# Performance work log

Hardware: AMD Instinct MI355X
Metric: run time of the kernel (lower is better)

Reference implementation:

```python
import jax, jax.numpy as jnp
import numpy as np

B, T, L, H, W, D = 16, 4096, 4, 128, 128, 32  # batch, points, views, plane HxW, c_dim
MAX_DIM = 0.55


def _linear_init(key, fan_in, fan_out):
    k1, k2 = jax.random.split(key)
    bound = 1.0 / np.sqrt(fan_in)
    Wm = jax.random.uniform(k1, (fan_in, fan_out), minval=-bound, maxval=bound, dtype=jnp.float32)
    b = jax.random.uniform(k2, (fan_out,), minval=-bound, maxval=bound, dtype=jnp.float32)
    return Wm, b


def setup_inputs() -> dict:
    key = jax.random.key(0)
    ks = jax.random.split(key, 10)
    p = jax.random.uniform(ks[0], (B, T, 3), dtype=jnp.float32, minval=-0.5, maxval=0.5)
    z = jax.random.normal(ks[1], (B, 128), dtype=jnp.float32)
    c = jax.random.normal(ks[2], (B, L, H, W, D), dtype=jnp.float32)
    C_mat = jax.random.normal(ks[3], (B, L, 4, 3), dtype=jnp.float32)
    fc_p_W, fc_p_b = _linear_init(ks[4], 3, D)
    # 5 ResnetBlockFC blocks, each with fc_0 and fc_1 (D->D)
    W0s, b0s, W1s, b1s = [], [], [], []
    for i in range(5):
        kk = jax.random.split(ks[5 + (i % 4)], 2 * (i + 1))
        w0, bb0 = _linear_init(jax.random.fold_in(key, 100 + i), D, D)
        w1, bb1 = _linear_init(jax.random.fold_in(key, 200 + i), D, D)
        W0s.append(w0); b0s.append(bb0); W1s.append(w1); b1s.append(bb1)
    blocks_W0 = jnp.stack(W0s); blocks_b0 = jnp.stack(b0s)
    blocks_W1 = jnp.stack(W1s); blocks_b1 = jnp.stack(b1s)
    fc_out_W, fc_out_b = _linear_init(ks[9], D, 1)
    return {
        'p': p, 'z': z, 'c': c, 'C_mat': C_mat,
        'fc_p_W': fc_p_W, 'fc_p_b': fc_p_b,
        'blocks_W0': blocks_W0, 'blocks_b0': blocks_b0,
        'blocks_W1': blocks_W1, 'blocks_b1': blocks_b1,
        'fc_out_W': fc_out_W, 'fc_out_b': fc_out_b,
    }


def bilinear_interpolation(p, net, C_mat):
    # p: [B,T,3]; net: [B,L,H,W,D]; C_mat: [B,L,4,3]
    Bb, Ll, Hh, Ww, Dd = net.shape
    interval = 2.0 / (Hh - 1)
    # project points with all views at once: C[:, l, :3] @ p^T, vectorized over l
    proj = jnp.einsum('blij,btj->blti', C_mat[:, :, :3, :], p / MAX_DIM)  # [B,L,T,3]
    proj = proj / (C_mat[:, :, 3, 0] + 0.05)[:, :, None, None]
    xy = (proj[..., :2] + 1.0) / interval  # [B,L,T,2]
    xy = jnp.where(xy >= Hh - 1, Hh - 1 - 0.1, xy)
    xy = jnp.where(xy < 0, 0.0, xy)
    xg, yg = xy[..., 0], xy[..., 1]  # [B,L,T]
    # torch.round and jnp.round both round half-to-even
    xl = jnp.round(xg - 0.5); xr = jnp.round(xg + 0.5)
    yl = jnp.round(yg - 0.5); yh = jnp.round(yg + 0.5)
    xi_l = xl.astype(jnp.int32); xi_r = xr.astype(jnp.int32)
    yi_l = yl.astype(jnp.int32); yi_h = yh.astype(jnp.int32)
    bi = jnp.arange(Bb)[:, None, None]
    li = jnp.arange(Ll)[None, :, None]
    f11 = net[bi, li, xi_l, yi_l]  # [B,L,T,D]
    f12 = net[bi, li, xi_r, yi_l]
    f21 = net[bi, li, xi_l, yi_h]
    f22 = net[bi, li, xi_r, yi_h]
    dx = (xr - xg)[..., None]
    dy = (yh - yg)[..., None]
    feat = f11 * dx * dy + f12 * (1 - dx) * dy + f21 * dx * (1 - dy) + f22 * (1 - dx) * (1 - dy)
    return jnp.sum(feat, axis=1)  # sum over views -> [B,T,D]


def resnet_block(x, W0, b0, W1, b1):
    # ResnetBlockFC(size_in == size_out): x + fc_1(relu(fc_0(relu(x))))
    h = jax.nn.relu(x) @ W0 + b0
    dx = jax.nn.relu(h) @ W1 + b1
    return x + dx


def reference(p, z, c, C_mat, fc_p_W, fc_p_b, blocks_W0, blocks_b0, blocks_W1, blocks_b1, fc_out_W, fc_out_b):
    cf = bilinear_interpolation(p, c, C_mat)  # [B,T,D]
    net = p @ fc_p_W + fc_p_b  # [B,T,D]
    net = net + cf
    net = resnet_block(net, blocks_W0[0], blocks_b0[0], blocks_W1[0], blocks_b1[0])
    for i in range(1, 5):
        net = net + cf
        net = resnet_block(net, blocks_W0[i], blocks_b0[i], blocks_W1[i], blocks_b1[i])
    out = jax.nn.relu(net) @ fc_out_W + fc_out_b  # [B,T,1]
    return out[..., 0]
```

## Files before the change

kernel.cpp:

```cpp
#include <hip/hip_runtime.h>
#include <hip/hip_bf16.h>


#define LL 4
#define HH 128
#define WW 128
#define DD 32
#define NPT 65536

typedef __attribute__((ext_vector_type(8))) short bf16x8t;
typedef __attribute__((ext_vector_type(4))) float f32x4;

union ABfrag { bf16x8t v; unsigned u[4]; };

__device__ __forceinline__ unsigned pk2(float a, float b) {
    __hip_bfloat16 ha = __float2bfloat16(a);
    __hip_bfloat16 hb = __float2bfloat16(b);
    unsigned short ua = *reinterpret_cast<unsigned short*>(&ha);
    unsigned short ub = *reinterpret_cast<unsigned short*>(&hb);
    return (unsigned)ua | ((unsigned)ub << 16);
}

__global__ __launch_bounds__(512, 2) void decoder_fused_mfma(
    const float* __restrict__ p,
    const float* __restrict__ c,
    const float* __restrict__ Cmat,
    const float* __restrict__ fc_p_W,
    const float* __restrict__ fc_p_b,
    const float* __restrict__ W0,
    const float* __restrict__ b0,
    const float* __restrict__ W1,
    const float* __restrict__ b1,
    const float* __restrict__ fc_out_W,
    const float* __restrict__ fc_out_b,
    float* __restrict__ out)
{
    __shared__ float xb[4608];

    const int tid = threadIdx.x;

    const int i    = blockIdx.x;
    const int b_u  = (i & 7) + ((i >> 8) << 3);
    const int blk  = (i >> 3) & 31;
    const int tbase = b_u * 4096 + blk * 128;

    const float inv_maxdim   = 1.0f / 0.55f;
    const float inv_interval = 1.0f / (float)(2.0 / 127.0);

    {
        const int tl = tid >> 2;
        const int dg = tid & 3;
        const int t  = tbase + tl;

        const float* pp = p + (size_t)t * 3;
        const float pm0 = pp[0] * inv_maxdim;
        const float pm1 = pp[1] * inv_maxdim;
        const float pm2 = pp[2] * inv_maxdim;

        float acc[8];
        #pragma unroll
        for (int ii = 0; ii < 8; ++ii) acc[ii] = 0.0f;

        #pragma unroll
        for (int l = 0; l < LL; ++l) {
            const float* cm = Cmat + (size_t)(b_u * LL + l) * 12;
            const float c00 = cm[0], c01 = cm[1], c02 = cm[2];
            const float c10 = cm[3], c11 = cm[4], c12 = cm[5];
            const float c30 = cm[9];

            float pr0 = c00 * pm0 + c01 * pm1 + c02 * pm2;
            float pr1 = c10 * pm0 + c11 * pm1 + c12 * pm2;
            const float denom = c30 + 0.05f;
            pr0 = pr0 / denom;
            pr1 = pr1 / denom;

            float xg = (pr0 + 1.0f) * inv_interval;
            float yg = (pr1 + 1.0f) * inv_interval;
            xg = (xg >= 127.0f) ? 126.9f : xg;
            xg = (xg < 0.0f)    ? 0.0f   : xg;
            yg = (yg >= 127.0f) ? 126.9f : yg;
            yg = (yg < 0.0f)    ? 0.0f   : yg;

            const float xl = rintf(xg - 0.5f);
            const float xr = rintf(xg + 0.5f);
            const float yl = rintf(yg - 0.5f);
            const float yh = rintf(yg + 0.5f);
            const int xil = (int)xl, xir = (int)xr, yil = (int)yl, yih = (int)yh;

            const float dx = xr - xg;
            const float dy = yh - yg;
            const float w11 = dx * dy;
            const float w12 = (1.0f - dx) * dy;
            const float w21 = dx * (1.0f - dy);
            const float w22 = (1.0f - dx) * (1.0f - dy);

            const float* plane = c + (size_t)(b_u * LL + l) * (HH * WW * DD);
            const int doff = dg * 8;
            const float* t11 = plane + ((size_t)xil * WW + yil) * DD + doff;
            const float* t12 = plane + ((size_t)xir * WW + yil) * DD + doff;
            const float* t21 = plane + ((size_t)xil * WW + yih) * DD + doff;
            const float* t22 = plane + ((size_t)xir * WW + yih) * DD + doff;

            #pragma unroll
            for (int hf = 0; hf < 2; ++hf) {
                const float4 a  = *(const float4*)(t11 + 4 * hf);
                const float4 e  = *(const float4*)(t12 + 4 * hf);
                const float4 g  = *(const float4*)(t21 + 4 * hf);
                const float4 d4 = *(const float4*)(t22 + 4 * hf);
                acc[4*hf + 0] += w11 * a.x + w12 * e.x + w21 * g.x + w22 * d4.x;
                acc[4*hf + 1] += w11 * a.y + w12 * e.y + w21 * g.y + w22 * d4.y;
                acc[4*hf + 2] += w11 * a.z + w12 * e.z + w21 * g.z + w22 * d4.z;
                acc[4*hf + 3] += w11 * a.w + w12 * e.w + w21 * g.w + w22 * d4.w;
            }
        }

        float* dst = xb + tl * 36 + dg * 8;
        *(float4*)(dst)     = make_float4(acc[0], acc[1], acc[2], acc[3]);
        *(float4*)(dst + 4) = make_float4(acc[4], acc[5], acc[6], acc[7]);
    }
    __syncthreads();

    const int lane = tid & 63;
    const int wv   = tid >> 6;
    const int cch  = lane & 15;
    const int q    = lane >> 4;
    const int tl0  = wv * 16;
    const int tpt  = tbase + tl0;

    f32x4 cf0, cf1;
    #pragma unroll
    for (int r = 0; r < 4; ++r) {
        const int ptl = tl0 + q * 4 + r;
        cf0[r] = xb[ptl * 36 + cch];
        cf1[r] = xb[ptl * 36 + 16 + cch];
    }

    const float fpb0 = fc_p_b[cch],        fpb1 = fc_p_b[16 + cch];
    const float fw00 = fc_p_W[cch],        fw01 = fc_p_W[16 + cch];
    const float fw10 = fc_p_W[DD + cch],   fw11 = fc_p_W[DD + 16 + cch];
    const float fw20 = fc_p_W[2*DD + cch], fw21 = fc_p_W[2*DD + 16 + cch];

    f32x4 net0, net1;
    #pragma unroll
    for (int r = 0; r < 4; ++r) {
        const int pt = tpt + q * 4 + r;
        const float* pp = p + (size_t)pt * 3;
        const float px = pp[0], py = pp[1], pz = pp[2];
        net0[r] = fpb0 + px * fw00 + py * fw10 + pz * fw20 + cf0[r];
        net1[r] = fpb1 + px * fw01 + py * fw11 + pz * fw21 + cf1[r];
    }

    __syncthreads();
    float* myxb = xb + wv * 576;

    #pragma unroll
    for (int s = 0; s < 5; ++s) {
        unsigned wB[2][2][4];
        #pragma unroll
        for (int m = 0; m < 2; ++m) {
            const float* Wm = (m ? W1 : W0) + s * DD * DD;
            #pragma unroll
            for (int tile = 0; tile < 2; ++tile) {
                const float* base = Wm + tile * 16 + cch;
                #pragma unroll
                for (int ii = 0; ii < 4; ++ii) {
                    const float wlo = base[(8 * q + 2 * ii)     * DD];
                    const float whi = base[(8 * q + 2 * ii + 1) * DD];
                    wB[m][tile][ii] = pk2(wlo, whi);
                }
            }
        }
        const float bc00 = b0[s * DD + cch];
        const float bc01 = b0[s * DD + 16 + cch];
        const float bc10 = b1[s * DD + cch];
        const float bc11 = b1[s * DD + 16 + cch];

        if (s > 0) {
            #pragma unroll
            for (int r = 0; r < 4; ++r) { net0[r] += cf0[r]; net1[r] += cf1[r]; }
        }

        #pragma unroll
        for (int r = 0; r < 4; ++r) {
            myxb[(q * 4 + r) * 36 + cch]      = fmaxf(net0[r], 0.0f);
            myxb[(q * 4 + r) * 36 + 16 + cch] = fmaxf(net1[r], 0.0f);
        }
        __syncthreads();
        ABfrag A1;
        {
            const float* row = myxb + cch * 36 + 8 * q;
            const f32x4 alo = *(const f32x4*)(row);
            const f32x4 ahi = *(const f32x4*)(row + 4);
            A1.u[0] = pk2(alo[0], alo[1]);
            A1.u[1] = pk2(alo[2], alo[3]);
            A1.u[2] = pk2(ahi[0], ahi[1]);
            A1.u[3] = pk2(ahi[2], ahi[3]);
        }
        __syncthreads();

        f32x4 h0 = { bc00, bc00, bc00, bc00 };
        f32x4 h1 = { bc01, bc01, bc01, bc01 };
        {
            ABfrag B0a, B0b;
            #pragma unroll
            for (int ii = 0; ii < 4; ++ii) { B0a.u[ii] = wB[0][0][ii]; B0b.u[ii] = wB[0][1][ii]; }
            h0 = __builtin_amdgcn_mfma_f32_16x16x32_bf16(A1.v, B0a.v, h0, 0, 0, 0);
            h1 = __builtin_amdgcn_mfma_f32_16x16x32_bf16(A1.v, B0b.v, h1, 0, 0, 0);
        }

        #pragma unroll
        for (int r = 0; r < 4; ++r) {
            myxb[(q * 4 + r) * 36 + cch]      = fmaxf(h0[r], 0.0f);
            myxb[(q * 4 + r) * 36 + 16 + cch] = fmaxf(h1[r], 0.0f);
        }
        __syncthreads();
        ABfrag A2;
        {
            const float* row = myxb + cch * 36 + 8 * q;
            const f32x4 alo = *(const f32x4*)(row);
            const f32x4 ahi = *(const f32x4*)(row + 4);
            A2.u[0] = pk2(alo[0], alo[1]);
            A2.u[1] = pk2(alo[2], alo[3]);
            A2.u[2] = pk2(ahi[0], ahi[1]);
            A2.u[3] = pk2(ahi[2], ahi[3]);
        }
        __syncthreads();

        #pragma unroll
        for (int r = 0; r < 4; ++r) { net0[r] += bc10; net1[r] += bc11; }
        {
            ABfrag B1a, B1b;
            #pragma unroll
            for (int ii = 0; ii < 4; ++ii) { B1a.u[ii] = wB[1][0][ii]; B1b.u[ii] = wB[1][1][ii]; }
            net0 = __builtin_amdgcn_mfma_f32_16x16x32_bf16(A2.v, B1a.v, net0, 0, 0, 0);
            net1 = __builtin_amdgcn_mfma_f32_16x16x32_bf16(A2.v, B1b.v, net1, 0, 0, 0);
        }
    }

    const float wo0 = fc_out_W[cch];
    const float wo1 = fc_out_W[16 + cch];
    float acc[4];
    #pragma unroll
    for (int r = 0; r < 4; ++r)
        acc[r] = fmaxf(net0[r], 0.0f) * wo0 + fmaxf(net1[r], 0.0f) * wo1;
    #pragma unroll
    for (int m = 1; m < 16; m <<= 1) {
        #pragma unroll
        for (int r = 0; r < 4; ++r) acc[r] += __shfl_xor(acc[r], m, 64);
    }
    if (cch == 0) {
        const float ob = fc_out_b[0];
        #pragma unroll
        for (int r = 0; r < 4; ++r) out[tpt + q * 4 + r] = acc[r] + ob;
    }
}

extern "C" void kernel_launch(void* const* d_in, const int* in_sizes, int n_in,
                              void* d_out, int out_size, void* d_ws, size_t ws_size,
                              hipStream_t stream) {
    const float* p        = (const float*)d_in[0];
    const float* c        = (const float*)d_in[2];
    const float* Cmat     = (const float*)d_in[3];
    const float* fc_p_W   = (const float*)d_in[4];
    const float* fc_p_b   = (const float*)d_in[5];
    const float* W0       = (const float*)d_in[6];
    const float* b0       = (const float*)d_in[7];
    const float* W1       = (const float*)d_in[8];
    const float* b1       = (const float*)d_in[9];
    const float* fc_out_W = (const float*)d_in[10];
    const float* fc_out_b = (const float*)d_in[11];
    float* out = (float*)d_out;

    decoder_fused_mfma<<<NPT / 128, 512, 0, stream>>>(p, c, Cmat, fc_p_W, fc_p_b,
                                                      W0, b0, W1, b1, fc_out_W, fc_out_b, out);
}
```

Measured before the change: 208.0 us.

## Stage packed MLP weights in LDS and replace block barriers with wave-local fences

The bf16-packed weight fragments and biases for all five residual blocks are now built once per workgroup into shared-memory tables, instead of every wave re-reading and re-packing them from global memory at each stage. The scaled point coordinates are also cached in shared memory, so the fc_p step no longer reloads p from global memory. Each stage's block-wide __syncthreads pairs become a single s_waitcnt lgkmcnt(0). This relies on each wave touching only its own 16-row slice of the scratch buffer. The cost is extra LDS (about 23 KB of tables), which may limit occupancy, and the correctness depends on wave-local LDS ordering.

```diff
diff --git a/kernel.cpp b/kernel.cpp
--- a/kernel.cpp
+++ b/kernel.cpp
@@ -19,6 +19,10 @@
     unsigned short ua = *reinterpret_cast<unsigned short*>(&ha);
     unsigned short ub = *reinterpret_cast<unsigned short*>(&hb);
     return (unsigned)ua | ((unsigned)ub << 16);
+}
+
+__device__ __forceinline__ void lds_fence() {
+    asm volatile("s_waitcnt lgkmcnt(0)" ::: "memory");
 }
 
 __global__ __launch_bounds__(512, 2) void decoder_fused_mfma(
@@ -35,7 +39,9 @@
     const float* __restrict__ fc_out_b,
     float* __restrict__ out)
 {
-    __shared__ float xb[4608];
+    __shared__ __align__(16) float xb[4608];
+    __shared__ uint4 wtab[1280];
+    __shared__ float btab[640];
 
     const int tid = threadIdx.x;
 
@@ -47,6 +53,25 @@
     const float inv_maxdim   = 1.0f / 0.55f;
     const float inv_interval = 1.0f / (float)(2.0 / 127.0);
 
+    for (int f = tid; f < 1280; f += 512) {
+        const int ln   = f & 63;
+        const int idx  = f >> 6;
+        const int tile = idx & 1;
+        const int m    = (idx >> 1) & 1;
+        const int s    = idx >> 2;
+        const int cchf = ln & 15;
+        const int qf   = ln >> 4;
+        const float* base = (m ? W1 : W0) + s * DD * DD + tile * 16 + cchf;
+        uint4 w;
+        w.x = pk2(base[(8 * qf + 0) * DD], base[(8 * qf + 1) * DD]);
+        w.y = pk2(base[(8 * qf + 2) * DD], base[(8 * qf + 3) * DD]);
+        w.z = pk2(base[(8 * qf + 4) * DD], base[(8 * qf + 5) * DD]);
+        w.w = pk2(base[(8 * qf + 6) * DD], base[(8 * qf + 7) * DD]);
+        wtab[f] = w;
+    }
+    for (int f = tid; f < 640; f += 512)
+        btab[f] = (f < 320) ? b0[f] : b1[f - 320];
+
     {
         const int tl = tid >> 2;
         const int dg = tid & 3;
@@ -56,6 +81,12 @@
         const float pm0 = pp[0] * inv_maxdim;
         const float pm1 = pp[1] * inv_maxdim;
         const float pm2 = pp[2] * inv_maxdim;
+
+        if (dg == 0) {
+            xb[tl * 36 + 32] = pm0;
+            xb[tl * 36 + 33] = pm1;
+            xb[tl * 36 + 34] = pm2;
+        }
 
         float acc[8];
         #pragma unroll
@@ -118,6 +149,7 @@
         *(float4*)(dst)     = make_float4(acc[0], acc[1], acc[2], acc[3]);
         *(float4*)(dst + 4) = make_float4(acc[4], acc[5], acc[6], acc[7]);
     }
+
     __syncthreads();
 
     const int lane = tid & 63;
@@ -135,45 +167,30 @@
         cf1[r] = xb[ptl * 36 + 16 + cch];
     }
 
-    const float fpb0 = fc_p_b[cch],        fpb1 = fc_p_b[16 + cch];
-    const float fw00 = fc_p_W[cch],        fw01 = fc_p_W[16 + cch];
-    const float fw10 = fc_p_W[DD + cch],   fw11 = fc_p_W[DD + 16 + cch];
-    const float fw20 = fc_p_W[2*DD + cch], fw21 = fc_p_W[2*DD + 16 + cch];
+    const float fpb0 = fc_p_b[cch],                fpb1 = fc_p_b[16 + cch];
+    const float fw00 = fc_p_W[cch] * 0.55f,        fw01 = fc_p_W[16 + cch] * 0.55f;
+    const float fw10 = fc_p_W[DD + cch] * 0.55f,   fw11 = fc_p_W[DD + 16 + cch] * 0.55f;
+    const float fw20 = fc_p_W[2*DD + cch] * 0.55f, fw21 = fc_p_W[2*DD + 16 + cch] * 0.55f;
 
     f32x4 net0, net1;
     #pragma unroll
     for (int r = 0; r < 4; ++r) {
-        const int pt = tpt + q * 4 + r;
-        const float* pp = p + (size_t)pt * 3;
-        const float px = pp[0], py = pp[1], pz = pp[2];
+        const int ptl = tl0 + q * 4 + r;
+        const float px = xb[ptl * 36 + 32];
+        const float py = xb[ptl * 36 + 33];
+        const float pz = xb[ptl * 36 + 34];
         net0[r] = fpb0 + px * fw00 + py * fw10 + pz * fw20 + cf0[r];
         net1[r] = fpb1 + px * fw01 + py * fw11 + pz * fw21 + cf1[r];
     }
 
-    __syncthreads();
     float* myxb = xb + wv * 576;
 
     #pragma unroll
     for (int s = 0; s < 5; ++s) {
-        unsigned wB[2][2][4];
-        #pragma unroll
-        for (int m = 0; m < 2; ++m) {
-            const float* Wm = (m ? W1 : W0) + s * DD * DD;
-            #pragma unroll
-            for (int tile = 0; tile < 2; ++tile) {
-                const float* base = Wm + tile * 16 + cch;
-                #pragma unroll
-                for (int ii = 0; ii < 4; ++ii) {
-                    const float wlo = base[(8 * q + 2 * ii)     * DD];
-                    const float whi = base[(8 * q + 2 * ii + 1) * DD];
-                    wB[m][tile][ii] = pk2(wlo, whi);
-                }
-            }
-        }
-        const float bc00 = b0[s * DD + cch];
-        const float bc01 = b0[s * DD + 16 + cch];
-        const float bc10 = b1[s * DD + cch];
-        const float bc11 = b1[s * DD + 16 + cch];
+        const float bc00 = btab[s * DD + cch];
+        const float bc01 = btab[s * DD + 16 + cch];
+        const float bc10 = btab[320 + s * DD + cch];
+        const float bc11 = btab[320 + s * DD + 16 + cch];
 
         if (s > 0) {
             #pragma unroll
@@ -185,7 +202,7 @@
             myxb[(q * 4 + r) * 36 + cch]      = fmaxf(net0[r], 0.0f);
             myxb[(q * 4 + r) * 36 + 16 + cch] = fmaxf(net1[r], 0.0f);
         }
-        __syncthreads();
+        lds_fence();
         ABfrag A1;
         {
             const float* row = myxb + cch * 36 + 8 * q;
@@ -196,14 +213,15 @@
             A1.u[2] = pk2(ahi[0], ahi[1]);
             A1.u[3] = pk2(ahi[2], ahi[3]);
         }
-        __syncthreads();
 
         f32x4 h0 = { bc00, bc00, bc00, bc00 };
         f32x4 h1 = { bc01, bc01, bc01, bc01 };
         {
             ABfrag B0a, B0b;
-            #pragma unroll
-            for (int ii = 0; ii < 4; ++ii) { B0a.u[ii] = wB[0][0][ii]; B0b.u[ii] = wB[0][1][ii]; }
+            const uint4 wa = wtab[(s * 4 + 0) * 64 + lane];
+            const uint4 wb = wtab[(s * 4 + 1) * 64 + lane];
+            B0a.u[0] = wa.x; B0a.u[1] = wa.y; B0a.u[2] = wa.z; B0a.u[3] = wa.w;
+            B0b.u[0] = wb.x; B0b.u[1] = wb.y; B0b.u[2] = wb.z; B0b.u[3] = wb.w;
             h0 = __builtin_amdgcn_mfma_f32_16x16x32_bf16(A1.v, B0a.v, h0, 0, 0, 0);
             h1 = __builtin_amdgcn_mfma_f32_16x16x32_bf16(A1.v, B0b.v, h1, 0, 0, 0);
         }
@@ -213,7 +231,7 @@
             myxb[(q * 4 + r) * 36 + cch]      = fmaxf(h0[r], 0.0f);
             myxb[(q * 4 + r) * 36 + 16 + cch] = fmaxf(h1[r], 0.0f);
         }
-        __syncthreads();
+        lds_fence();
         ABfrag A2;
         {
             const float* row = myxb + cch * 36 + 8 * q;
@@ -224,14 +242,15 @@
             A2.u[2] = pk2(ahi[0], ahi[1]);
             A2.u[3] = pk2(ahi[2], ahi[3]);
         }
-        __syncthreads();
 
         #pragma unroll
         for (int r = 0; r < 4; ++r) { net0[r] += bc10; net1[r] += bc11; }
         {
             ABfrag B1a, B1b;
-            #pragma unroll
-            for (int ii = 0; ii < 4; ++ii) { B1a.u[ii] = wB[1][0][ii]; B1b.u[ii] = wB[1][1][ii]; }
+            const uint4 wa = wtab[(s * 4 + 2) * 64 + lane];
+            const uint4 wb = wtab[(s * 4 + 3) * 64 + lane];
+            B1a.u[0] = wa.x; B1a.u[1] = wa.y; B1a.u[2] = wa.z; B1a.u[3] = wa.w;
+            B1b.u[0] = wb.x; B1b.u[1] = wb.y; B1b.u[2] = wb.z; B1b.u[3] = wb.w;
             net0 = __builtin_amdgcn_mfma_f32_16x16x32_bf16(A2.v, B1a.v, net0, 0, 0, 0);
             net1 = __builtin_amdgcn_mfma_f32_16x16x32_bf16(A2.v, B1b.v, net1, 0, 0, 0);
         }
```

Result: faster. 203.5 us (-2.1%).
